# Optimization experiments

Hardware: AMD Instinct MI355X
Metric: run time of the kernel (lower is better)

Reference implementation:

```python
import jax, jax.numpy as jnp
import numpy as np

K = 20
EPS = 1e-5  # BatchNorm eps, eval mode with running_mean=0, running_var=1


def _bn(x, g, b):
    # eval-mode BatchNorm with running stats (mean=0, var=1): affine only
    return x * (g / jnp.sqrt(1.0 + EPS)) + b


def _lrelu(x):
    return jax.nn.leaky_relu(x, 0.2)


def setup_inputs() -> dict:
    key = jax.random.key(0)
    ks = jax.random.split(key, 8)
    B, N, EMB, OUT = 8, 4096, 1024, 128
    def w(k, shape):
        fan_in = shape[0]
        return (jax.random.normal(k, shape, jnp.float32) / np.sqrt(fan_in)).astype(jnp.float32)
    inp = {
        "x":  jax.random.normal(ks[0], (B, N, 3), jnp.float32),
        "W1": w(ks[1], (6, 64)),   "g1": jnp.ones(64),  "b1": jnp.zeros(64),
        "W2": w(ks[2], (64, 64)),  "g2": jnp.ones(64),  "b2": jnp.zeros(64),
        "W3": w(ks[3], (64, 128)), "g3": jnp.ones(128), "b3": jnp.zeros(128),
        "W4": w(ks[4], (128, 256)),"g4": jnp.ones(256), "b4": jnp.zeros(256),
        "W5": w(ks[5], (512, EMB)),"g5": jnp.ones(EMB), "b5": jnp.zeros(EMB),
        "L1": w(ks[6], (2 * EMB, 512)), "g6": jnp.ones(512), "b6": jnp.zeros(512),
        "L2": w(ks[7], (512, 256)), "L2b": jnp.zeros(256), "g7": jnp.ones(256), "b7": jnp.zeros(256),
        "L3": w(jax.random.fold_in(key, 99), (256, OUT)), "L3b": jnp.zeros(OUT),
    }
    return inp


def _knn_idx(pts):
    # pts: [B, 3, N]; returns indices of K nearest neighbors [B, N, K]
    inner = -2.0 * jnp.einsum('bdn,bdm->bnm', pts, pts)  # [B,N,N]
    xx = jnp.sum(pts * pts, axis=1)                       # [B,N]
    pd = -xx[:, :, None] - inner - xx[:, None, :]          # negative squared distance
    return jax.lax.top_k(pd, K)[1]                         # [B,N,K]


def reference(x, W1, g1, b1, W2, g2, b2, W3, g3, b3, W4, g4, b4,
              W5, g5, b5, L1, g6, b6, L2, L2b, g7, b7, L3, L3b):
    B, N, _ = x.shape
    pts = jnp.transpose(x, (0, 2, 1))           # [B,3,N]
    idx = _knn_idx(pts)                          # [B,N,K]

    # gather neighbor coordinates: [B,N,K,3]
    feature = jax.vmap(lambda xb, ib: xb[ib])(x, idx)
    center = jnp.broadcast_to(x[:, :, None, :], (B, N, K, 3))
    h = jnp.concatenate([feature, center], axis=-1)  # [B,N,K,6]

    h = _lrelu(_bn(jnp.einsum('bnkc,co->bnko', h, W1), g1, b1))
    x1 = jnp.max(h, axis=2)                          # [B,N,64]
    h = _lrelu(_bn(jnp.einsum('bnkc,co->bnko', h, W2), g2, b2))
    x2 = jnp.max(h, axis=2)                          # [B,N,64]
    h = _lrelu(_bn(jnp.einsum('bnkc,co->bnko', h, W3), g3, b3))
    x3 = jnp.max(h, axis=2)                          # [B,N,128]
    h = _lrelu(_bn(jnp.einsum('bnkc,co->bnko', h, W4), g4, b4))
    x4 = jnp.max(h, axis=2)                          # [B,N,256]

    hc = jnp.concatenate([x1, x2, x3, x4], axis=-1)  # [B,N,512]
    h5 = _lrelu(_bn(jnp.einsum('bnc,co->bno', hc, W5), g5, b5))  # [B,N,EMB]

    gmax = jnp.max(h5, axis=1)                       # [B,EMB]
    gavg = jnp.mean(h5, axis=1)                      # [B,EMB]
    g = jnp.concatenate([gmax, gavg], axis=-1)       # [B,2*EMB]

    f = _lrelu(_bn(g @ L1, g6, b6))                  # dropout = identity (eval)
    f = _lrelu(_bn(f @ L2 + L2b, g7, b7))
    return f @ L3 + L3b                              # [B,OUT]
```

## Files before the change

kernel.cpp:

```cpp
#include <hip/hip_runtime.h>
#include <hip/hip_bf16.h>
#include <hip/hip_fp16.h>

#define NPTS 4096
#define KNB  20
#define EPSB 1e-5f

typedef _Float16 half8 __attribute__((ext_vector_type(8)));
typedef float    f32x4 __attribute__((ext_vector_type(4)));

__device__ __forceinline__ f32x4 mfma16(half8 a, half8 b, f32x4 c){
  return __builtin_amdgcn_mfma_f32_16x16x32_f16(a, b, c, 0, 0, 0);
}

__device__ __forceinline__ half8 loadA_lds(const _Float16* buf, int C, int mt, int ks, int lane){
  int row = mt*16 + (lane & 15);
  int k0  = ks*32 + (lane >> 4)*8;
  int e   = (row*C + k0) ^ ((row & 7) << 3);
  return *reinterpret_cast<const half8*>(&buf[e]);
}

__device__ __forceinline__ half8 loadB_g(const _Float16* WT, int K, int nt, int ks, int lane){
  int col = nt*16 + (lane & 15);
  int k0  = ks*32 + (lane >> 4)*8;
  return *reinterpret_cast<const half8*>(&WT[col*K + k0]);
}

__global__ __launch_bounds__(1024)
void knn_kernel(const float* __restrict__ x, int* __restrict__ idx_out){
  __shared__ float4 spts[NPTS];
  int b  = blockIdx.x >> 8;
  int r0 = (blockIdx.x & 255) << 4;
  const float* xb = x + (size_t)b*NPTS*3;
  for (int t = threadIdx.x; t < NPTS; t += 1024){
    float px = xb[t*3+0], py = xb[t*3+1], pz = xb[t*3+2];
    spts[t] = make_float4(px, py, pz, px*px + py*py + pz*pz);
  }
  __syncthreads();
  int wave = threadIdx.x >> 6, lane = threadIdx.x & 63;
  int i = r0 + wave;
  float4 pi = spts[i];
  float b1 = -INFINITY, b2 = -INFINITY, b3 = -INFINITY;
  int   i1 = 0, i2 = 0, i3 = 0;
  #pragma unroll 8
  for (int t = 0; t < 64; ++t){
    int j = (t << 6) + lane;
    float4 q = spts[j];
    float d = 2.f*(pi.x*q.x + pi.y*q.y + pi.z*q.z) - pi.w - q.w;
    if (d > b1){ b3=b2; i3=i2; b2=b1; i2=i1; b1=d; i1=j; }
    else if (d > b2){ b3=b2; i3=i2; b2=d; i2=j; }
    else if (d > b3){ b3=d; i3=j; }
  }
  unsigned long long rem = 0ull;
  size_t obase = ((size_t)b*NPTS + i)*KNB;
  #pragma unroll 1
  for (int kk = 0; kk < KNB; ++kk){
    float bv = b1; int bi = i1;
    #pragma unroll
    for (int m = 32; m > 0; m >>= 1){
      float ov = __shfl_xor(bv, m);
      int   oi = __shfl_xor(bi, m);
      if (ov > bv || (ov == bv && oi < bi)){ bv = ov; bi = oi; }
    }
    if (lane == 0) idx_out[obase + kk] = bi;
    if ((bi & 63) == lane){
      rem |= 1ull << (bi >> 6);
      b1 = b2; i1 = i2; b2 = b3; i2 = i3; b3 = -INFINITY; i3 = 0;
      if (b1 == -INFINITY){
        #pragma unroll 8
        for (int t = 0; t < 64; ++t){
          if (rem & (1ull << t)) continue;
          int j = (t << 6) + lane;
          float4 q = spts[j];
          float d = 2.f*(pi.x*q.x + pi.y*q.y + pi.z*q.z) - pi.w - q.w;
          if (d > b1){ b3=b2; i3=i2; b2=b1; i2=i1; b1=d; i1=j; }
          else if (d > b2){ b3=b2; i3=i2; b2=d; i2=j; }
          else if (d > b3){ b3=d; i3=j; }
        }
      }
    }
  }
}

__global__ __launch_bounds__(256)
void prep_kernel(const float* __restrict__ W2, const float* __restrict__ W3,
                 const float* __restrict__ W4, const float* __restrict__ W5,
                 _Float16* __restrict__ W2T, _Float16* __restrict__ W3T,
                 _Float16* __restrict__ W4T, _Float16* __restrict__ W5T){
  int t = blockIdx.x*256 + threadIdx.x;
  if (t < 4096){ int o=t>>6, k=t&63;                W2T[t] = (_Float16)W2[k*64+o]; }
  else if (t < 12288){ int u=t-4096;  int o=u>>6, k=u&63;   W3T[u] = (_Float16)W3[k*128+o]; }
  else if (t < 45056){ int u=t-12288; int o=u>>7, k=u&127;  W4T[u] = (_Float16)W4[k*256+o]; }
  else if (t < 569344){ int u=t-45056; int o=u>>9, k=u&511; W5T[u] = (_Float16)W5[k*1024+o]; }
}

__device__ __forceinline__ void bucket(int mt, bool c1, bool c2, bool c3, float v,
                                       float& p0, float& p1, float& p2, float& p3){
  if (mt == 0)      p0 = fmaxf(p0, v);
  else if (mt == 4) p3 = fmaxf(p3, v);
  else if (mt == 1){ p1 = fmaxf(p1, c1 ? v : -INFINITY); p0 = fmaxf(p0, c1 ? -INFINITY : v); }
  else if (mt == 2){ p2 = fmaxf(p2, c2 ? v : -INFINITY); p1 = fmaxf(p1, c2 ? -INFINITY : v); }
  else             { p3 = fmaxf(p3, c3 ? v : -INFINITY); p2 = fmaxf(p2, c3 ? -INFINITY : v); }
}

__device__ __forceinline__ void reduce_write_x(float p0, float p1, float p2, float p3,
                                               _Float16* __restrict__ hc, size_t gp0,
                                               int off, int g, int c){
  p0 = fmaxf(p0, __shfl_xor(p0, 16)); p0 = fmaxf(p0, __shfl_xor(p0, 32));
  p1 = fmaxf(p1, __shfl_xor(p1, 16)); p1 = fmaxf(p1, __shfl_xor(p1, 32));
  p2 = fmaxf(p2, __shfl_xor(p2, 16)); p2 = fmaxf(p2, __shfl_xor(p2, 32));
  p3 = fmaxf(p3, __shfl_xor(p3, 16)); p3 = fmaxf(p3, __shfl_xor(p3, 32));
  float v = (g == 0) ? p0 : (g == 1) ? p1 : (g == 2) ? p2 : p3;
  hc[(gp0 + g)*512 + off + c] = (_Float16)v;
}

__global__ __launch_bounds__(256)
void edge_kernel(const float* __restrict__ x, const int* __restrict__ knn,
                 const float* __restrict__ W1, const float* __restrict__ g1, const float* __restrict__ b1,
                 const _Float16* __restrict__ W2T, const float* __restrict__ g2, const float* __restrict__ b2,
                 const _Float16* __restrict__ W3T, const float* __restrict__ g3, const float* __restrict__ b3,
                 const _Float16* __restrict__ W4T, const float* __restrict__ g4, const float* __restrict__ b4,
                 _Float16* __restrict__ hc){
  __shared__ __align__(16) char smem[40960];
  _Float16* hb1 = (_Float16*)(smem);
  _Float16* hb2 = (_Float16*)(smem + 10240);
  _Float16* hb3 = (_Float16*)(smem + 20480);
  float*    h0f = (float*)(smem + 20480);
  float*    h0c = (float*)(smem + 20480 + 1280);
  const float rs = 1.f / sqrtf(1.f + EPSB);
  int gp0 = blockIdx.x << 2;
  int b   = gp0 >> 12;
  int n0  = gp0 & (NPTS-1);
  const float* xb = x + (size_t)b*NPTS*3;
  int tid = threadIdx.x;
  if (tid < 80){
    int p = tid / 20, k = tid % 20;
    int nb = knn[((size_t)b*NPTS + n0 + p)*KNB + k];
    h0f[tid*4+0] = xb[nb*3+0];
    h0f[tid*4+1] = xb[nb*3+1];
    h0f[tid*4+2] = xb[nb*3+2];
  } else if (tid < 96){
    int u = tid - 80; int p = u >> 2, c = u & 3;
    if (c < 3) h0c[p*4+c] = xb[(n0+p)*3+c];
  }
  __syncthreads();
  int w = tid >> 6, lane = tid & 63, g = lane >> 4, cc = lane & 15;
  bool c1 = (g >= 1), c2 = (g >= 2), c3 = (g >= 3);
  {
    int col = lane;
    float sc = g1[col]*rs, bs = b1[col];
    float w0=W1[col], w1_=W1[64+col], w2_=W1[128+col], w3_=W1[192+col], w4_=W1[256+col], w5_=W1[320+col];
    float cx = h0c[w*4+0], cy = h0c[w*4+1], cz = h0c[w*4+2];
    float m1 = -INFINITY;
    #pragma unroll 5
    for (int k = 0; k < KNB; ++k){
      int r = w*20 + k;
      float a = h0f[r*4+0]*w0 + h0f[r*4+1]*w1_ + h0f[r*4+2]*w2_ + cx*w3_ + cy*w4_ + cz*w5_;
      float vv = a*sc + bs; vv = vv > 0.f ? vv : 0.2f*vv;
      hb1[((r<<6)+col) ^ ((r&7)<<3)] = (_Float16)vv;
      m1 = fmaxf(m1, vv);
    }
    hc[(size_t)(gp0 + w)*512 + col] = (_Float16)m1;
  }
  __syncthreads();
  {
    int colg = (w<<4) + cc;
    float sc = g2[colg]*rs, bs = b2[colg];
    half8 bf0 = loadB_g(W2T, 64, w, 0, lane);
    half8 bf1 = loadB_g(W2T, 64, w, 1, lane);
    float p0=-INFINITY, p1=-INFINITY, p2=-INFINITY, p3=-INFINITY;
    #pragma unroll
    for (int mt = 0; mt < 5; ++mt){
      f32x4 a = {0.f,0.f,0.f,0.f};
      a = mfma16(loadA_lds(hb1,64,mt,0,lane), bf0, a);
      a = mfma16(loadA_lds(hb1,64,mt,1,lane), bf1, a);
      #pragma unroll
      for (int rr = 0; rr < 4; ++rr){
        int row = mt*16 + g*4 + rr;
        float vv = a[rr]*sc + bs; vv = vv > 0.f ? vv : 0.2f*vv;
        hb2[(row*64 + colg) ^ ((row&7)<<3)] = (_Float16)vv;
        bucket(mt, c1, c2, c3, vv, p0, p1, p2, p3);
      }
    }
    reduce_write_x(p0,p1,p2,p3, hc, gp0, 64 + (w<<4), g, cc);
  }
  __syncthreads();
  {
    int ntA = (w<<1), ntB = ntA + 1;
    int colA = (ntA<<4) + cc, colB = (ntB<<4) + cc;
    float scA = g3[colA]*rs, bsA = b3[colA];
    float scB = g3[colB]*rs, bsB = b3[colB];
    half8 bA0 = loadB_g(W3T, 64, ntA, 0, lane);
    half8 bA1 = loadB_g(W3T, 64, ntA, 1, lane);
    half8 bB0 = loadB_g(W3T, 64, ntB, 0, lane);
    half8 bB1 = loadB_g(W3T, 64, ntB, 1, lane);
    float pA0=-INFINITY,pA1=-INFINITY,pA2=-INFINITY,pA3=-INFINITY;
    float pB0=-INFINITY,pB1=-INFINITY,pB2=-INFINITY,pB3=-INFINITY;
    #pragma unroll
    for (int mt = 0; mt < 5; ++mt){
      half8 a0 = loadA_lds(hb2,64,mt,0,lane);
      half8 a1 = loadA_lds(hb2,64,mt,1,lane);
      f32x4 aA = {0.f,0.f,0.f,0.f};
      aA = mfma16(a0, bA0, aA); aA = mfma16(a1, bA1, aA);
      f32x4 aB = {0.f,0.f,0.f,0.f};
      aB = mfma16(a0, bB0, aB); aB = mfma16(a1, bB1, aB);
      #pragma unroll
      for (int rr = 0; rr < 4; ++rr){
        int row = mt*16 + g*4 + rr;
        float vA = aA[rr]*scA + bsA; vA = vA > 0.f ? vA : 0.2f*vA;
        hb3[(row*128 + colA) ^ ((row&7)<<3)] = (_Float16)vA;
        bucket(mt, c1, c2, c3, vA, pA0, pA1, pA2, pA3);
        float vB = aB[rr]*scB + bsB; vB = vB > 0.f ? vB : 0.2f*vB;
        hb3[(row*128 + colB) ^ ((row&7)<<3)] = (_Float16)vB;
        bucket(mt, c1, c2, c3, vB, pB0, pB1, pB2, pB3);
      }
    }
    reduce_write_x(pA0,pA1,pA2,pA3, hc, gp0, 128 + (ntA<<4), g, cc);
    reduce_write_x(pB0,pB1,pB2,pB3, hc, gp0, 128 + (ntB<<4), g, cc);
  }
  __syncthreads();
  #pragma unroll 1
  for (int pass = 0; pass < 2; ++pass){
    int ntA = (pass<<3) + w, ntB = ntA + 4;
    int colA = (ntA<<4) + cc, colB = (ntB<<4) + cc;
    float scA = g4[colA]*rs, bsA = b4[colA];
    float scB = g4[colB]*rs, bsB = b4[colB];
    half8 bwA[4], bwB[4];
    #pragma unroll
    for (int ks = 0; ks < 4; ++ks){
      bwA[ks] = loadB_g(W4T, 128, ntA, ks, lane);
      bwB[ks] = loadB_g(W4T, 128, ntB, ks, lane);
    }
    float pA0=-INFINITY,pA1=-INFINITY,pA2=-INFINITY,pA3=-INFINITY;
    float pB0=-INFINITY,pB1=-INFINITY,pB2=-INFINITY,pB3=-INFINITY;
    #pragma unroll
    for (int mt = 0; mt < 5; ++mt){
      half8 a[4];
      #pragma unroll
      for (int ks = 0; ks < 4; ++ks) a[ks] = loadA_lds(hb3,128,mt,ks,lane);
      f32x4 aA = {0.f,0.f,0.f,0.f};
      #pragma unroll
      for (int ks = 0; ks < 4; ++ks) aA = mfma16(a[ks], bwA[ks], aA);
      f32x4 aB = {0.f,0.f,0.f,0.f};
      #pragma unroll
      for (int ks = 0; ks < 4; ++ks) aB = mfma16(a[ks], bwB[ks], aB);
      #pragma unroll
      for (int rr = 0; rr < 4; ++rr){
        float vA = aA[rr]*scA + bsA; vA = vA > 0.f ? vA : 0.2f*vA;
        bucket(mt, c1, c2, c3, vA, pA0, pA1, pA2, pA3);
        float vB = aB[rr]*scB + bsB; vB = vB > 0.f ? vB : 0.2f*vB;
        bucket(mt, c1, c2, c3, vB, pB0, pB1, pB2, pB3);
      }
    }
    reduce_write_x(pA0,pA1,pA2,pA3, hc, gp0, 256 + (ntA<<4), g, cc);
    reduce_write_x(pB0,pB1,pB2,pB3, hc, gp0, 256 + (ntB<<4), g, cc);
  }
}

__global__ __launch_bounds__(256)
void gemm5_kernel(const _Float16* __restrict__ hc, const _Float16* __restrict__ W5T,
                  const float* __restrict__ g5, const float* __restrict__ b5,
                  float* __restrict__ red){
  __shared__ __align__(16) _Float16 sA[64*512];
  int rowblk = blockIdx.x >> 2;
  int colblk = blockIdx.x & 3;
  int row0 = rowblk << 6;
  #pragma unroll 1
  for (int it = 0; it < 16; ++it){
    int eoff = it*2048 + threadIdx.x*8;
    int row = eoff >> 9;
    int ine = eoff & 511;
    half8 vsrc = *reinterpret_cast<const half8*>(
        &hc[(size_t)(row0 + row)*512 + (ine ^ ((row & 7) << 3))]);
    *reinterpret_cast<half8*>(&sA[(row << 9) + ine]) = vsrc;
  }
  __syncthreads();
  int wave = threadIdx.x >> 6, lane = threadIdx.x & 63;
  f32x4 acc[4][4] = {};
  #pragma unroll 1
  for (int ks = 0; ks < 16; ++ks){
    half8 af[4];
    #pragma unroll
    for (int mt = 0; mt < 4; ++mt) af[mt] = loadA_lds(sA, 512, mt, ks, lane);
    #pragma unroll
    for (int nt = 0; nt < 4; ++nt){
      int ntg = (colblk<<4) + (wave<<2) + nt;
      half8 bf = loadB_g(W5T, 512, ntg, ks, lane);
      #pragma unroll
      for (int mt = 0; mt < 4; ++mt)
        acc[mt][nt] = mfma16(af[mt], bf, acc[mt][nt]);
    }
  }
  int batch = row0 >> 12;
  int chunk = (row0 & (NPTS-1)) >> 6;
  const float rs = 1.f/sqrtf(1.f+EPSB);
  #pragma unroll
  for (int nt = 0; nt < 4; ++nt){
    int ntg = (colblk<<4) + (wave<<2) + nt;
    int colg = (ntg<<4) + (lane & 15);
    float sc = g5[colg]*rs, bs = b5[colg];
    float vmax = -INFINITY, vsum = 0.f;
    #pragma unroll
    for (int mt = 0; mt < 4; ++mt){
      #pragma unroll
      for (int r = 0; r < 4; ++r){
        float vv = acc[mt][nt][r]*sc + bs;
        vv = vv>0.f ? vv : 0.2f*vv;
        vmax = fmaxf(vmax, vv); vsum += vv;
      }
    }
    vmax = fmaxf(vmax, __shfl_xor(vmax, 16)); vsum += __shfl_xor(vsum, 16);
    vmax = fmaxf(vmax, __shfl_xor(vmax, 32)); vsum += __shfl_xor(vsum, 32);
    if ((lane >> 4) == 0){
      size_t base = (size_t)((batch<<6) + chunk)*2048;
      red[base + colg] = vmax;
      red[base + 1024 + colg] = vsum;
    }
  }
}

__global__ __launch_bounds__(256)
void reduce_g_kernel(const float* __restrict__ red, float* __restrict__ g){
  int t = blockIdx.x*256 + threadIdx.x;
  int b = t >> 10, col = t & 1023;
  float m = -INFINITY, s = 0.f;
  #pragma unroll 4
  for (int c = 0; c < 64; ++c){
    size_t base = (size_t)((b<<6)+c)*2048;
    m = fmaxf(m, red[base + col]);
    s += red[base + 1024 + col];
  }
  g[(b<<11) + col]        = m;
  g[(b<<11) + 1024 + col] = s * (1.f/4096.f);
}

__global__ __launch_bounds__(256)
void fc1_kernel(const float* __restrict__ g, const float* __restrict__ L1,
                const float* __restrict__ g6, const float* __restrict__ b6,
                float* __restrict__ f1){
  __shared__ float part[4][64];
  int b  = blockIdx.x >> 3;
  int og = blockIdx.x & 7;
  int o  = (og << 6) + (threadIdx.x & 63);
  int kg = threadIdx.x >> 6;
  const float* gb = g + (b << 11);
  float acc = 0.f;
  #pragma unroll 8
  for (int k = kg*512; k < kg*512 + 512; ++k) acc += gb[k]*L1[k*512 + o];
  part[kg][threadIdx.x & 63] = acc;
  __syncthreads();
  if (threadIdx.x < 64){
    float s = part[0][threadIdx.x] + part[1][threadIdx.x] + part[2][threadIdx.x] + part[3][threadIdx.x];
    float v = s*(g6[o]/sqrtf(1.f+EPSB)) + b6[o];
    f1[(b<<9) + o] = v > 0.f ? v : 0.2f*v;
  }
}

__global__ __launch_bounds__(256)
void fc2_kernel(const float* __restrict__ f1, const float* __restrict__ L2, const float* __restrict__ L2b,
                const float* __restrict__ g7, const float* __restrict__ b7, float* __restrict__ f2){
  __shared__ float part[4][64];
  int b  = blockIdx.x >> 2;
  int og = blockIdx.x & 3;
  int o  = (og << 6) + (threadIdx.x & 63);
  int kg = threadIdx.x >> 6;
  const float* fb = f1 + (b << 9);
  float acc = 0.f;
  #pragma unroll 8
  for (int k = kg*128; k < kg*128 + 128; ++k) acc += fb[k]*L2[k*256 + o];
  part[kg][threadIdx.x & 63] = acc;
  __syncthreads();
  if (threadIdx.x < 64){
    float s = part[0][threadIdx.x] + part[1][threadIdx.x] + part[2][threadIdx.x] + part[3][threadIdx.x];
    float v = (s + L2b[o])*(g7[o]/sqrtf(1.f+EPSB)) + b7[o];
    f2[(b<<8) + o] = v > 0.f ? v : 0.2f*v;
  }
}

__global__ __launch_bounds__(256)
void fc3_kernel(const float* __restrict__ f2, const float* __restrict__ L3, const float* __restrict__ L3b,
                float* __restrict__ out){
  __shared__ float part[2][128];
  int b  = blockIdx.x;
  int o  = threadIdx.x & 127;
  int kg = threadIdx.x >> 7;
  const float* fb = f2 + (b << 8);
  float acc = 0.f;
  #pragma unroll 8
  for (int k = kg*128; k < kg*128 + 128; ++k) acc += fb[k]*L3[k*128 + o];
  part[kg][o] = acc;
  __syncthreads();
  if (threadIdx.x < 128)
    out[(b<<7) + o] = part[0][o] + part[1][o] + L3b[o];
}

extern "C" void kernel_launch(void* const* d_in, const int* in_sizes, int n_in,
                              void* d_out, int out_size, void* d_ws, size_t ws_size,
                              hipStream_t stream){
  const float* x  = (const float*)d_in[0];
  const float* W1 = (const float*)d_in[1];
  const float* g1 = (const float*)d_in[2];  const float* b1 = (const float*)d_in[3];
  const float* W2 = (const float*)d_in[4];
  const float* g2 = (const float*)d_in[5];  const float* b2 = (const float*)d_in[6];
  const float* W3 = (const float*)d_in[7];
  const float* g3 = (const float*)d_in[8];  const float* b3 = (const float*)d_in[9];
  const float* W4 = (const float*)d_in[10];
  const float* g4 = (const float*)d_in[11]; const float* b4 = (const float*)d_in[12];
  const float* W5 = (const float*)d_in[13];
  const float* g5 = (const float*)d_in[14]; const float* b5 = (const float*)d_in[15];
  const float* L1 = (const float*)d_in[16];
  const float* g6 = (const float*)d_in[17]; const float* b6 = (const float*)d_in[18];
  const float* L2 = (const float*)d_in[19]; const float* L2b = (const float*)d_in[20];
  const float* g7 = (const float*)d_in[21]; const float* b7 = (const float*)d_in[22];
  const float* L3 = (const float*)d_in[23]; const float* L3b = (const float*)d_in[24];

  char* ws = (char*)d_ws;
  int*      idx  = (int*)(ws + 0);
  _Float16* hc   = (_Float16*)(ws + 2621440);
  _Float16* W2T  = (_Float16*)(ws + 36175872);
  _Float16* W3T  = (_Float16*)(ws + 36184064);
  _Float16* W4T  = (_Float16*)(ws + 36200448);
  _Float16* W5T  = (_Float16*)(ws + 36265984);
  float*    red  = (float*)(ws + 37314560);
  float*    gbuf = (float*)(ws + 41508864);
  float*    f1   = (float*)(ws + 41574400);
  float*    f2   = (float*)(ws + 41590784);

  knn_kernel<<<2048, 1024, 0, stream>>>(x, idx);
  prep_kernel<<<2224, 256, 0, stream>>>(W2, W3, W4, W5, W2T, W3T, W4T, W5T);
  edge_kernel<<<8192, 256, 0, stream>>>(x, idx, W1, g1, b1, W2T, g2, b2,
                                        W3T, g3, b3, W4T, g4, b4, hc);
  gemm5_kernel<<<2048, 256, 0, stream>>>(hc, W5T, g5, b5, red);
  reduce_g_kernel<<<32, 256, 0, stream>>>(red, gbuf);
  fc1_kernel<<<64, 256, 0, stream>>>(gbuf, L1, g6, b6, f1);
  fc2_kernel<<<32, 256, 0, stream>>>(f1, L2, L2b, g7, b7, f2);
  fc3_kernel<<<8, 256, 0, stream>>>(f2, L3, L3b, (float*)d_out);
}
```

Baseline: 474.5 us.

## Branchless kNN top-3 insertion, faster warp argmax, tiled W5 transpose

The kNN distance now uses a pre-halved squared norm, which drops the multiply by 2, and the per-lane top-3 insertion is rewritten branch-free with fmax/fmin and selects. The wave argmax reduces only the value with shuffles, then resolves the index with a ballot, and runs an extra min-reduction only when values tie. The refill check becomes wave-uniform and is skipped on the last round. The W5 transpose moves to its own LDS-tiled kernel so both its reads and writes are coalesced. The scaled distances change the tie-break only in rare floating-point cases.

```diff
diff --git a/kernel.cpp b/kernel.cpp
--- a/kernel.cpp
+++ b/kernel.cpp
@@ -34,7 +34,7 @@
   const float* xb = x + (size_t)b*NPTS*3;
   for (int t = threadIdx.x; t < NPTS; t += 1024){
     float px = xb[t*3+0], py = xb[t*3+1], pz = xb[t*3+2];
-    spts[t] = make_float4(px, py, pz, px*px + py*py + pz*pz);
+    spts[t] = make_float4(px, py, pz, 0.5f*(px*px + py*py + pz*pz));
   }
   __syncthreads();
   int wave = threadIdx.x >> 6, lane = threadIdx.x & 63;
@@ -46,36 +46,58 @@
   for (int t = 0; t < 64; ++t){
     int j = (t << 6) + lane;
     float4 q = spts[j];
-    float d = 2.f*(pi.x*q.x + pi.y*q.y + pi.z*q.z) - pi.w - q.w;
-    if (d > b1){ b3=b2; i3=i2; b2=b1; i2=i1; b1=d; i1=j; }
-    else if (d > b2){ b3=b2; i3=i2; b2=d; i2=j; }
-    else if (d > b3){ b3=d; i3=j; }
+    float d = pi.x*q.x + pi.y*q.y + pi.z*q.z - pi.w - q.w;
+    bool c1 = d > b1, c2 = d > b2, c3 = d > b3;
+    float t2 = fmaxf(b2, fminf(b1, d));
+    float t3 = fmaxf(b3, fminf(b2, d));
+    i3 = c2 ? i2 : (c3 ? j : i3);
+    i2 = c1 ? i1 : (c2 ? j : i2);
+    i1 = c1 ? j : i1;
+    b1 = fmaxf(b1, d);
+    b2 = t2; b3 = t3;
   }
   unsigned long long rem = 0ull;
   size_t obase = ((size_t)b*NPTS + i)*KNB;
   #pragma unroll 1
   for (int kk = 0; kk < KNB; ++kk){
-    float bv = b1; int bi = i1;
-    #pragma unroll
-    for (int m = 32; m > 0; m >>= 1){
-      float ov = __shfl_xor(bv, m);
-      int   oi = __shfl_xor(bi, m);
-      if (ov > bv || (ov == bv && oi < bi)){ bv = ov; bi = oi; }
-    }
-    if (lane == 0) idx_out[obase + kk] = bi;
-    if ((bi & 63) == lane){
-      rem |= 1ull << (bi >> 6);
-      b1 = b2; i1 = i2; b2 = b3; i2 = i3; b3 = -INFINITY; i3 = 0;
+    float bv = b1;
+    #pragma unroll
+    for (int m = 1; m <= 32; m <<= 1)
+      bv = fmaxf(bv, __shfl_xor(bv, m));
+    unsigned long long tied = __ballot(b1 == bv);
+    int bj;
+    if (__popcll(tied) > 1){
+      int jv = (b1 == bv) ? i1 : 0x7fffffff;
+      #pragma unroll
+      for (int m = 1; m <= 32; m <<= 1)
+        jv = min(jv, __shfl_xor(jv, m));
+      bj = jv;
+    } else {
+      bj = __shfl(i1, (int)__ffsll(tied) - 1);
+    }
+    if (lane == 0) idx_out[obase + kk] = bj;
+    bool iwin = (b1 == bv) && (i1 == bj);
+    if (iwin){
+      rem |= 1ull << (i1 >> 6);
+      b1 = b2; i1 = i2; b2 = b3; i2 = i3; b3 = -INFINITY;
+    }
+    if (kk < KNB-1 && __any(b1 == -INFINITY)){
       if (b1 == -INFINITY){
+        b2 = -INFINITY; b3 = -INFINITY; i1 = 0; i2 = 0; i3 = 0;
         #pragma unroll 8
         for (int t = 0; t < 64; ++t){
           if (rem & (1ull << t)) continue;
           int j = (t << 6) + lane;
           float4 q = spts[j];
-          float d = 2.f*(pi.x*q.x + pi.y*q.y + pi.z*q.z) - pi.w - q.w;
-          if (d > b1){ b3=b2; i3=i2; b2=b1; i2=i1; b1=d; i1=j; }
-          else if (d > b2){ b3=b2; i3=i2; b2=d; i2=j; }
-          else if (d > b3){ b3=d; i3=j; }
+          float d = pi.x*q.x + pi.y*q.y + pi.z*q.z - pi.w - q.w;
+          bool c1 = d > b1, c2 = d > b2, c3 = d > b3;
+          float t2 = fmaxf(b2, fminf(b1, d));
+          float t3 = fmaxf(b3, fminf(b2, d));
+          i3 = c2 ? i2 : (c3 ? j : i3);
+          i2 = c1 ? i1 : (c2 ? j : i2);
+          i1 = c1 ? j : i1;
+          b1 = fmaxf(b1, d);
+          b2 = t2; b3 = t3;
         }
       }
     }
@@ -84,14 +106,29 @@
 
 __global__ __launch_bounds__(256)
 void prep_kernel(const float* __restrict__ W2, const float* __restrict__ W3,
-                 const float* __restrict__ W4, const float* __restrict__ W5,
+                 const float* __restrict__ W4,
                  _Float16* __restrict__ W2T, _Float16* __restrict__ W3T,
-                 _Float16* __restrict__ W4T, _Float16* __restrict__ W5T){
+                 _Float16* __restrict__ W4T){
   int t = blockIdx.x*256 + threadIdx.x;
   if (t < 4096){ int o=t>>6, k=t&63;                W2T[t] = (_Float16)W2[k*64+o]; }
   else if (t < 12288){ int u=t-4096;  int o=u>>6, k=u&63;   W3T[u] = (_Float16)W3[k*128+o]; }
   else if (t < 45056){ int u=t-12288; int o=u>>7, k=u&127;  W4T[u] = (_Float16)W4[k*256+o]; }
-  else if (t < 569344){ int u=t-45056; int o=u>>9, k=u&511; W5T[u] = (_Float16)W5[k*1024+o]; }
+}
+
+__global__ __launch_bounds__(256)
+void prep5_kernel(const float* __restrict__ W5, _Float16* __restrict__ W5T){
+  __shared__ float tile[32][33];
+  int tk = (blockIdx.x & 15) << 5;
+  int to = (blockIdx.x >> 4) << 5;
+  int lr = threadIdx.x >> 5;
+  int lc = threadIdx.x & 31;
+  #pragma unroll
+  for (int r = 0; r < 32; r += 8)
+    tile[lr + r][lc] = W5[(size_t)(tk + lr + r)*1024 + to + lc];
+  __syncthreads();
+  #pragma unroll
+  for (int r = 0; r < 32; r += 8)
+    W5T[(size_t)(to + lr + r)*512 + tk + lc] = (_Float16)tile[lc][lr + r];
 }
 
 __device__ __forceinline__ void bucket(int mt, bool c1, bool c2, bool c3, float v,
@@ -427,7 +464,8 @@
   float*    f2   = (float*)(ws + 41590784);
 
   knn_kernel<<<2048, 1024, 0, stream>>>(x, idx);
-  prep_kernel<<<2224, 256, 0, stream>>>(W2, W3, W4, W5, W2T, W3T, W4T, W5T);
+  prep_kernel<<<176, 256, 0, stream>>>(W2, W3, W4, W2T, W3T, W4T);
+  prep5_kernel<<<512, 256, 0, stream>>>(W5, W5T);
   edge_kernel<<<8192, 256, 0, stream>>>(x, idx, W1, g1, b1, W2T, g2, b2,
                                         W3T, g3, b3, W4T, g4, b4, hc);
   gemm5_kernel<<<2048, 256, 0, stream>>>(hc, W5T, g5, b5, red);
```

New measurement: 437.8 us. 7.7% less time.
